# Optimization experiments

Hardware: AMD Instinct MI355X
Metric: run time of the kernel (lower is better)

Reference implementation:

```python
import math
import jax, jax.numpy as jnp
import numpy as np

B, T, C, H = 4, 1024, 1024, 16


def setup_inputs() -> dict:
    key = jax.random.key(0)
    k1, k2, k3 = jax.random.split(key, 3)
    scale = 0.02
    return {
        "x": jax.random.normal(k1, (B, T, C), dtype=jnp.float32),
        "w_attn": jax.random.normal(k2, (C, 3 * C), dtype=jnp.float32) * scale,
        "b_attn": jnp.zeros((3 * C,), dtype=jnp.float32),
        "w_proj": jax.random.normal(k3, (C, C), dtype=jnp.float32) * scale,
        "b_proj": jnp.zeros((C,), dtype=jnp.float32),
    }


def reference(x, w_attn, b_attn, w_proj, b_proj):
    b, t, c = x.shape
    h = H
    d = c // h
    qkv = x @ w_attn + b_attn                      # [b, t, 3c]
    q, k, v = jnp.split(qkv, 3, axis=-1)
    # [b, h, t, d]
    q = q.reshape(b, t, h, d).transpose(0, 2, 1, 3)
    k = k.reshape(b, t, h, d).transpose(0, 2, 1, 3)
    v = v.reshape(b, t, h, d).transpose(0, 2, 1, 3)
    att = jnp.einsum("bhqd,bhkd->bhqk", q, k) * (1.0 / math.sqrt(d))
    causal = jnp.tril(jnp.ones((t, t), dtype=bool))
    att = jnp.where(causal[None, None], att, -jnp.inf)
    att = jax.nn.softmax(att, axis=-1)
    # dropout is identity in eval mode
    y = jnp.einsum("bhqk,bhkd->bhqd", att, v)      # [b, h, t, d]
    y = y.transpose(0, 2, 1, 3).reshape(b, t, c)
    return y @ w_proj + b_proj
```

## Files before the change

### kernel.cpp

```cpp
#include <hip/hip_runtime.h>

typedef __bf16 bf16;
typedef float f32x4 __attribute__((ext_vector_type(4)));
typedef bf16 bf16x4 __attribute__((ext_vector_type(4)));
typedef bf16 bf16x8 __attribute__((ext_vector_type(8)));

#define MFMA16(a, b, c) __builtin_amdgcn_mfma_f32_16x16x32_bf16((a), (b), (c), 0, 0, 0)

__device__ __forceinline__ f32x4 zero4() {
    f32x4 z; z[0] = 0.f; z[1] = 0.f; z[2] = 0.f; z[3] = 0.f; return z;
}
__device__ __forceinline__ float max3f(float a, float b, float c) {
    return fmaxf(fmaxf(a, b), c);
}
__device__ __forceinline__ void gl_lds16(const bf16* g, bf16* l) {
    __builtin_amdgcn_global_load_lds(
        (const __attribute__((address_space(1))) void*)g,
        (__attribute__((address_space(3))) void*)l, 16, 0, 0);
}

__global__ __launch_bounds__(256)
void prep_k(const float* __restrict__ x, bf16* __restrict__ xb,
            const float* __restrict__ w_attn, bf16* __restrict__ wT,
            const float* __restrict__ w_proj, bf16* __restrict__ wpT)
{
    __shared__ bf16 Ls[64][72];
    const int blk = blockIdx.x;
    const int tid = threadIdx.x;

    if (blk < 2048) {
        const int i = (blk * 256 + tid) * 8;
        const float4 a = *(const float4*)(x + i);
        const float4 b = *(const float4*)(x + i + 4);
        bf16x8 o;
        o[0] = (bf16)a.x; o[1] = (bf16)a.y; o[2] = (bf16)a.z; o[3] = (bf16)a.w;
        o[4] = (bf16)b.x; o[5] = (bf16)b.y; o[6] = (bf16)b.z; o[7] = (bf16)b.w;
        *(bf16x8*)(xb + i) = o;
        return;
    }
    const float* src;
    bf16* dst;
    int K, N, bx, by;
    if (blk < 2816) {
        const int r = blk - 2048;
        src = w_attn; dst = wT; K = 1024; N = 3072;
        bx = r % 48; by = r / 48;
    } else {
        const int r = blk - 2816;
        src = w_proj; dst = wpT; K = 1024; N = 1024;
        bx = r & 15; by = r >> 4;
    }
    const int k0 = by << 6;
    const int n0 = bx << 6;
    #pragma unroll
    for (int it = 0; it < 4; ++it) {
        const int lin = (it << 10) + (tid << 2);
        const int r = lin >> 6, c = lin & 63;
        const float4 v = *(const float4*)(src + (size_t)(k0 + r) * N + n0 + c);
        bf16x4 o; o[0] = (bf16)v.x; o[1] = (bf16)v.y; o[2] = (bf16)v.z; o[3] = (bf16)v.w;
        *(bf16x4*)&Ls[r][c] = o;
    }
    __syncthreads();
    #pragma unroll
    for (int it = 0; it < 2; ++it) {
        const int lin = (it << 11) + (tid << 3);
        const int nn = lin >> 6, kk = lin & 63;
        bf16x8 o;
        #pragma unroll
        for (int j = 0; j < 8; ++j) o[j] = Ls[kk + j][nn];
        *(bf16x8*)(dst + (size_t)(n0 + nn) * K + k0 + kk) = o;
    }
}

template <int MODE>
__global__ __launch_bounds__(256)
void gemm_bt(const bf16* __restrict__ A, const bf16* __restrict__ Bt,
             const float* __restrict__ bias,
             bf16* __restrict__ qw, bf16* __restrict__ kw, bf16* __restrict__ vw,
             float* __restrict__ outf)
{
    constexpr int BK = 32;
    constexpr int BN = (MODE == 0) ? 128 : 64;
    constexpr int K  = 1024;
    constexpr int N  = (MODE == 0) ? 3072 : 1024;
    constexpr int MF = (MODE == 0) ? 4 : 2;
    constexpr int NF = 4;
    constexpr int AE = 128 * BK;
    constexpr int BE = BN * BK;
    constexpr int nk = K / BK;

    __shared__ __align__(16) bf16 smem[3 * (AE + BE)];
    bf16* const Asb = smem;
    bf16* const Bsb = smem + 3 * AE;

    const int tid  = threadIdx.x;
    const int lane = tid & 63;
    const int wid  = tid >> 6;
    const int l16  = lane & 15;
    const int g    = lane >> 4;
    const int wrb  = (MODE == 0) ? ((wid >> 1) << 6) : (wid << 5);
    const int wcb  = (MODE == 0) ? ((wid & 1) << 6) : 0;

    const int p   = blockIdx.x;
    const int xcd = p & 7;
    const int r   = p >> 3;
    int by, bx;
    if (MODE == 0) { by = ((xcd >> 1) << 3) + r / 12; bx = (xcd & 1) * 12 + r % 12; }
    else           { by = ((xcd >> 1) << 3) + (r >> 3); bx = ((xcd & 1) << 3) + (r & 7); }
    const int m0 = by << 7;
    const int n0 = bx * BN;

    const int srow = lane >> 2;
    const int schk = lane & 3;
    const int rA0 = (wid << 5) + srow;
    const int rA1 = rA0 + 16;
    const int rB0 = wid * (BN / 4) + srow;
    const int rB1 = rB0 + 16;
    const bf16* const pa0 = A  + (size_t)(m0 + rA0) * K + ((schk ^ ((rA0 >> 1) & 3)) << 3);
    const bf16* const pa1 = A  + (size_t)(m0 + rA1) * K + ((schk ^ ((rA1 >> 1) & 3)) << 3);
    const bf16* const pb0 = Bt + (size_t)(n0 + rB0) * K + ((schk ^ ((rB0 >> 1) & 3)) << 3);
    const bf16* const pb1 = Bt + (size_t)(n0 + rB1) * K + ((schk ^ ((rB1 >> 1) & 3)) << 3);
    const int dA0 = (wid << 5) * BK, dA1 = dA0 + 16 * BK;
    const int dB0 = (wid * (BN / 4)) * BK, dB1 = dB0 + 16 * BK;

    int offA[MF], offB[NF];
    #pragma unroll
    for (int mf = 0; mf < MF; ++mf) {
        const int rr = wrb + (mf << 4) + l16;
        offA[mf] = rr * BK + ((g ^ ((rr >> 1) & 3)) << 3);
    }
    #pragma unroll
    for (int nf = 0; nf < NF; ++nf) {
        const int rr = wcb + (nf << 4) + l16;
        offB[nf] = rr * BK + ((g ^ ((rr >> 1) & 3)) << 3);
    }

    f32x4 acc[MF][NF];
    #pragma unroll
    for (int i = 0; i < MF; ++i)
        #pragma unroll
        for (int j = 0; j < NF; ++j) acc[i][j] = zero4();

    auto issue = [&](int t, int s) {
        bf16* const ab = Asb + s * AE;
        bf16* const bb = Bsb + s * BE;
        gl_lds16(pa0 + t * BK, ab + dA0);
        gl_lds16(pa1 + t * BK, ab + dA1);
        gl_lds16(pb0 + t * BK, bb + dB0);
        if constexpr (MODE == 0) gl_lds16(pb1 + t * BK, bb + dB1);
    };

    issue(0, 0);
    issue(1, 1);

    #pragma unroll
    for (int kt = 0; kt < nk; ++kt) {
        if (kt == nk - 1) {
            asm volatile("s_waitcnt vmcnt(0)" ::: "memory");
        } else {
            if constexpr (MODE == 0) asm volatile("s_waitcnt vmcnt(4)" ::: "memory");
            else                     asm volatile("s_waitcnt vmcnt(3)" ::: "memory");
        }
        __builtin_amdgcn_s_barrier();
        if (kt + 2 < nk) issue(kt + 2, (kt + 2) % 3);
        const bf16* const ac = Asb + (kt % 3) * AE;
        const bf16* const bc = Bsb + (kt % 3) * BE;
        bf16x8 af[MF], bfr[NF];
        #pragma unroll
        for (int mf = 0; mf < MF; ++mf) af[mf] = *(const bf16x8*)&ac[offA[mf]];
        #pragma unroll
        for (int nf = 0; nf < NF; ++nf) bfr[nf] = *(const bf16x8*)&bc[offB[nf]];
        __builtin_amdgcn_s_setprio(1);
        #pragma unroll
        for (int mf = 0; mf < MF; ++mf)
            #pragma unroll
            for (int nf = 0; nf < NF; ++nf)
                acc[mf][nf] = MFMA16(af[mf], bfr[nf], acc[mf][nf]);
        __builtin_amdgcn_s_setprio(0);
    }
    __syncthreads();

    if (MODE == 0) {
        bf16* const Es = smem;
        const int bq  = m0 >> 10;
        const int tb  = m0 & 1023;
        const int hh0 = (n0 & 1023) >> 6;
        const bool isV = (n0 >= 2048);
        if (isV) {
            #pragma unroll
            for (int mf = 0; mf < MF; ++mf)
                #pragma unroll
                for (int nf = 0; nf < NF; ++nf) {
                    const int nn = wcb + (nf << 4) + l16;
                    const float bs = bias[n0 + nn];
                    bf16x4 pq;
                    #pragma unroll
                    for (int j = 0; j < 4; ++j) pq[j] = (bf16)(acc[mf][nf][j] + bs);
                    const int m = wrb + (mf << 4) + (g << 2);
                    const int pp = ((m >> 5) << 5) + (((m >> 2) & 3) << 3) + (((m >> 4) & 1) << 2);
                    *(bf16x4*)&Es[nn * 128 + pp] = pq;
                }
        } else {
            #pragma unroll
            for (int mf = 0; mf < MF; ++mf)
                #pragma unroll
                for (int nf = 0; nf < NF; ++nf) {
                    const int nn = wcb + (nf << 4) + l16;
                    const float bs = bias[n0 + nn];
                    #pragma unroll
                    for (int j = 0; j < 4; ++j) {
                        const int mm = wrb + (mf << 4) + (g << 2) + j;
                        Es[mm * 128 + nn] = (bf16)(acc[mf][nf][j] + bs);
                    }
                }
        }
        __syncthreads();
        #pragma unroll
        for (int it = 0; it < 8; ++it) {
            const int idx = (it << 8) + tid;
            const int row = idx >> 4, ch = idx & 15;
            const bf16x8 v = *(const bf16x8*)&Es[row * 128 + (ch << 3)];
            if (isV) {
                const int dd = row & 63, hh = hh0 + (row >> 6);
                *(bf16x8*)(vw + ((size_t)((bq << 4) + hh) << 16) + ((size_t)dd << 10)
                           + tb + (ch << 3)) = v;
            } else {
                const int t = tb + row;
                const int cc = ch << 3;
                const int hh = hh0 + (cc >> 6);
                bf16* const dst = (n0 < 1024) ? qw : kw;
                *(bf16x8*)(dst + ((size_t)((bq << 4) + hh) << 16) + ((size_t)t << 6)
                           + (cc & 63)) = v;
            }
        }
    } else {
        #pragma unroll
        for (int mf = 0; mf < MF; ++mf)
            #pragma unroll
            for (int nf = 0; nf < NF; ++nf) {
                const int ng = n0 + wcb + (nf << 4) + l16;
                const float bs = bias[ng];
                #pragma unroll
                for (int j = 0; j < 4; ++j) {
                    const int mg = m0 + wrb + (mf << 4) + (g << 2) + j;
                    outf[(size_t)mg * N + ng] = acc[mf][nf][j] + bs;
                }
            }
    }
}

__global__ __launch_bounds__(256)
void attn_k(const bf16* __restrict__ Qp, const bf16* __restrict__ Kp,
            const bf16* __restrict__ Vt, bf16* __restrict__ att)
{
    __shared__ __align__(16) bf16 Kls[3 * 64 * 64];
    __shared__ __align__(16) bf16 Vls[3 * 64 * 64];

    const int bh = blockIdx.x;
    const int bx = blockIdx.y;
    const int b  = bh >> 4, h = bh & 15;

    const int tid  = threadIdx.x;
    const int lane = tid & 63;
    const int wid  = tid >> 6;
    const int g    = lane >> 4;
    const int l16  = lane & 15;
    const int g8   = g << 3;

    const size_t hb = (size_t)bh << 16;
    const bf16* Qh = Qp + hb;
    const bf16* Kh = Kp + hb;
    const bf16* Vh = Vt + hb;

    const int srow = lane >> 3;
    const int sswz = ((lane & 7) ^ srow) << 3;
    const int kr0  = (wid << 4) + srow;
    const int kr1  = kr0 + 8;
    const int dst0 = (wid << 4) << 6;
    const int dst1 = ((wid << 4) + 8) << 6;

    int offKV[2][4];
    #pragma unroll
    for (int ks = 0; ks < 2; ++ks)
        #pragma unroll
        for (int cb = 0; cb < 4; ++cb) {
            const int r = (cb << 4) + l16;
            offKV[ks][cb] = (r << 6) + (((((ks << 2) + g)) ^ (r & 7)) << 3);
        }

    const float QSCALE = 0.125f * 1.44269504f;

    const int q1b = bx;
    const int q2b = 15 - bx;
    const int nkt = q2b;
    const int qloc = (wid << 4) + l16;

    const bf16* qp1 = Qh + ((size_t)((q1b << 6) + qloc) << 6) + g8;
    const bf16* qp2 = Qh + ((size_t)((q2b << 6) + qloc) << 6) + g8;
    bf16x8 q1f0 = *(const bf16x8*)qp1, q1f1 = *(const bf16x8*)(qp1 + 32);
    bf16x8 q2f0 = *(const bf16x8*)qp2, q2f1 = *(const bf16x8*)(qp2 + 32);
    #pragma unroll
    for (int e = 0; e < 8; ++e) {
        q1f0[e] = (bf16)(QSCALE * (float)q1f0[e]);
        q1f1[e] = (bf16)(QSCALE * (float)q1f1[e]);
        q2f0[e] = (bf16)(QSCALE * (float)q2f0[e]);
        q2f1[e] = (bf16)(QSCALE * (float)q2f1[e]);
    }

    f32x4 acc1[4], acc2[4];
    float m1 = -1e30f, l1 = 0.f, m2 = -1e30f, l2 = 0.f;
    #pragma unroll
    for (int i = 0; i < 4; ++i) { acc1[i] = zero4(); acc2[i] = zero4(); }

    auto stage = [&](int t, int s) {
        const int kv = t << 6;
        bf16* const Kn = Kls + s * 4096;
        bf16* const Vn = Vls + s * 4096;
        gl_lds16(Kh + ((size_t)(kv + kr0) << 6) + sswz, Kn + dst0);
        gl_lds16(Kh + ((size_t)(kv + kr1) << 6) + sswz, Kn + dst1);
        gl_lds16(Vh + ((size_t)kr0 << 10) + kv + sswz, Vn + dst0);
        gl_lds16(Vh + ((size_t)kr1 << 10) + kv + sswz, Vn + dst1);
    };

    stage(0, 0);
    stage(1, 1);

    for (int kt = 0; kt <= nkt; ++kt) {
        const int slot = kt % 3;
        if (kt + 2 <= nkt) {
            stage(kt + 2, (kt + 2) % 3);
            asm volatile("s_waitcnt vmcnt(8)" ::: "memory");
        } else if (kt + 1 <= nkt) {
            asm volatile("s_waitcnt vmcnt(4)" ::: "memory");
        } else {
            asm volatile("s_waitcnt vmcnt(0)" ::: "memory");
        }
        __builtin_amdgcn_s_barrier();
        const bf16* Kc = Kls + slot * 4096;
        const bf16* Vc = Vls + slot * 4096;

        bf16x8 kf[2][4], vf[2][4];
        #pragma unroll
        for (int ks = 0; ks < 2; ++ks)
            #pragma unroll
            for (int cb = 0; cb < 4; ++cb) {
                kf[ks][cb] = *(const bf16x8*)&Kc[offKV[ks][cb]];
                vf[ks][cb] = *(const bf16x8*)&Vc[offKV[ks][cb]];
            }

        {
            f32x4 sacc[4];
            #pragma unroll
            for (int cb = 0; cb < 4; ++cb) sacc[cb] = zero4();
            #pragma unroll
            for (int cb = 0; cb < 4; ++cb) sacc[cb] = MFMA16(kf[0][cb], q2f0, sacc[cb]);
            #pragma unroll
            for (int cb = 0; cb < 4; ++cb) sacc[cb] = MFMA16(kf[1][cb], q2f1, sacc[cb]);
            if (kt == q2b) {
                #pragma unroll
                for (int cb = 0; cb < 4; ++cb)
                    #pragma unroll
                    for (int j = 0; j < 4; ++j)
                        if (((cb << 4) + (g << 2) + j) > qloc) sacc[cb][j] = -1e30f;
            }
            const float t0 = max3f(sacc[0][0], sacc[0][1], sacc[0][2]);
            const float t1 = max3f(sacc[0][3], sacc[1][0], sacc[1][1]);
            const float t2 = max3f(sacc[1][2], sacc[1][3], sacc[2][0]);
            const float t3 = max3f(sacc[2][1], sacc[2][2], sacc[2][3]);
            const float t4 = max3f(sacc[3][0], sacc[3][1], sacc[3][2]);
            float pm = fmaxf(max3f(t0, t1, t2), max3f(t3, t4, sacc[3][3]));
            pm = fmaxf(pm, __shfl_xor(pm, 16));
            pm = fmaxf(pm, __shfl_xor(pm, 32));
            if (__any(pm > m2 + 8.f)) {
                const float mn = fmaxf(m2, pm);
                const float sc = __builtin_amdgcn_exp2f(m2 - mn);
                m2 = mn; l2 *= sc;
                #pragma unroll
                for (int db = 0; db < 4; ++db)
                    #pragma unroll
                    for (int j = 0; j < 4; ++j) acc2[db][j] *= sc;
            }
            float rsum = 0.f;
            #pragma unroll
            for (int cb = 0; cb < 4; ++cb)
                #pragma unroll
                for (int j = 0; j < 4; ++j) {
                    const float pv = __builtin_amdgcn_exp2f(sacc[cb][j] - m2);
                    sacc[cb][j] = pv;
                    rsum += pv;
                }
            rsum += __shfl_xor(rsum, 16);
            rsum += __shfl_xor(rsum, 32);
            l2 += rsum;
            bf16x8 pf0, pf1;
            #pragma unroll
            for (int i = 0; i < 8; ++i) {
                pf0[i] = (bf16)sacc[i >> 2][i & 3];
                pf1[i] = (bf16)sacc[2 + (i >> 2)][i & 3];
            }
            #pragma unroll
            for (int db = 0; db < 4; ++db) acc2[db] = MFMA16(vf[0][db], pf0, acc2[db]);
            #pragma unroll
            for (int db = 0; db < 4; ++db) acc2[db] = MFMA16(vf[1][db], pf1, acc2[db]);
        }

        if (kt <= q1b) {
            f32x4 sacc[4];
            #pragma unroll
            for (int cb = 0; cb < 4; ++cb) sacc[cb] = zero4();
            #pragma unroll
            for (int cb = 0; cb < 4; ++cb) sacc[cb] = MFMA16(kf[0][cb], q1f0, sacc[cb]);
            #pragma unroll
            for (int cb = 0; cb < 4; ++cb) sacc[cb] = MFMA16(kf[1][cb], q1f1, sacc[cb]);
            if (kt == q1b) {
                #pragma unroll
                for (int cb = 0; cb < 4; ++cb)
                    #pragma unroll
                    for (int j = 0; j < 4; ++j)
                        if (((cb << 4) + (g << 2) + j) > qloc) sacc[cb][j] = -1e30f;
            }
            const float t0 = max3f(sacc[0][0], sacc[0][1], sacc[0][2]);
            const float t1 = max3f(sacc[0][3], sacc[1][0], sacc[1][1]);
            const float t2 = max3f(sacc[1][2], sacc[1][3], sacc[2][0]);
            const float t3 = max3f(sacc[2][1], sacc[2][2], sacc[2][3]);
            const float t4 = max3f(sacc[3][0], sacc[3][1], sacc[3][2]);
            float pm = fmaxf(max3f(t0, t1, t2), max3f(t3, t4, sacc[3][3]));
            pm = fmaxf(pm, __shfl_xor(pm, 16));
            pm = fmaxf(pm, __shfl_xor(pm, 32));
            if (__any(pm > m1 + 8.f)) {
                const float mn = fmaxf(m1, pm);
                const float sc = __builtin_amdgcn_exp2f(m1 - mn);
                m1 = mn; l1 *= sc;
                #pragma unroll
                for (int db = 0; db < 4; ++db)
                    #pragma unroll
                    for (int j = 0; j < 4; ++j) acc1[db][j] *= sc;
            }
            float rsum = 0.f;
            #pragma unroll
            for (int cb = 0; cb < 4; ++cb)
                #pragma unroll
                for (int j = 0; j < 4; ++j) {
                    const float pv = __builtin_amdgcn_exp2f(sacc[cb][j] - m1);
                    sacc[cb][j] = pv;
                    rsum += pv;
                }
            rsum += __shfl_xor(rsum, 16);
            rsum += __shfl_xor(rsum, 32);
            l1 += rsum;
            bf16x8 pf0, pf1;
            #pragma unroll
            for (int i = 0; i < 8; ++i) {
                pf0[i] = (bf16)sacc[i >> 2][i & 3];
                pf1[i] = (bf16)sacc[2 + (i >> 2)][i & 3];
            }
            #pragma unroll
            for (int db = 0; db < 4; ++db) acc1[db] = MFMA16(vf[0][db], pf0, acc1[db]);
            #pragma unroll
            for (int db = 0; db < 4; ++db) acc1[db] = MFMA16(vf[1][db], pf1, acc1[db]);
        }
        asm volatile("" ::: "memory");
        __builtin_amdgcn_s_barrier();
        asm volatile("" ::: "memory");
    }

    {
        const float inv = 1.f / l2;
        const int t = (q2b << 6) + qloc;
        #pragma unroll
        for (int db = 0; db < 4; ++db) {
            bf16x4 o;
            #pragma unroll
            for (int j = 0; j < 4; ++j) o[j] = (bf16)(acc2[db][j] * inv);
            *(bf16x4*)(att + (((size_t)b << 10) + t) * 1024 + (h << 6) + (db << 4) + (g << 2)) = o;
        }
    }
    {
        const float inv = 1.f / l1;
        const int t = (q1b << 6) + qloc;
        #pragma unroll
        for (int db = 0; db < 4; ++db) {
            bf16x4 o;
            #pragma unroll
            for (int j = 0; j < 4; ++j) o[j] = (bf16)(acc1[db][j] * inv);
            *(bf16x4*)(att + (((size_t)b << 10) + t) * 1024 + (h << 6) + (db << 4) + (g << 2)) = o;
        }
    }
}

extern "C" void kernel_launch(void* const* d_in, const int* in_sizes, int n_in,
                              void* d_out, int out_size, void* d_ws, size_t ws_size,
                              hipStream_t stream)
{
    const float* x      = (const float*)d_in[0];
    const float* w_attn = (const float*)d_in[1];
    const float* b_attn = (const float*)d_in[2];
    const float* w_proj = (const float*)d_in[3];
    const float* b_proj = (const float*)d_in[4];
    float* out = (float*)d_out;

    bf16* xb  = (bf16*)d_ws;
    bf16* wT  = xb  + (size_t)4096 * 1024;
    bf16* wpT = wT  + (size_t)3072 * 1024;
    bf16* qw  = wpT + (size_t)1024 * 1024;
    bf16* kw  = qw  + (size_t)64 * 1024 * 64;
    bf16* vw  = kw  + (size_t)64 * 1024 * 64;
    bf16* aw  = vw  + (size_t)64 * 1024 * 64;

    prep_k<<<3072, 256, 0, stream>>>(x, xb, w_attn, wT, w_proj, wpT);

    gemm_bt<0><<<768, 256, 0, stream>>>(xb, wT, b_attn, qw, kw, vw, nullptr);
    attn_k<<<dim3(64, 8), 256, 0, stream>>>(qw, kw, vw, aw);
    gemm_bt<1><<<512, 256, 0, stream>>>(aw, wpT, b_proj, nullptr, nullptr, nullptr, out);
}
```

Measured before the change: 84.76 us.

## Split paired causal query blocks into one block per CTA with XCD-aware mapping

The attention kernel previously had each CTA handle a pair of query blocks (bx and 15-bx) that shared the K/V tiles loaded into LDS. It now launches 1024 CTAs, each owning a single 64-row query block. The CTA index is remapped so that each XCD gets whole heads and the longest query blocks are scheduled first. The K/V ring shrinks from three LDS stages to double buffering, which cuts LDS per CTA and should allow more CTAs per CU. The cost is that every K/V tile is loaded twice as often, with less reuse per load, and there is more per-CTA setup overhead.

```diff
diff --git a/kernel.cpp b/kernel.cpp
--- a/kernel.cpp
+++ b/kernel.cpp
@@ -253,12 +253,18 @@
 void attn_k(const bf16* __restrict__ Qp, const bf16* __restrict__ Kp,
             const bf16* __restrict__ Vt, bf16* __restrict__ att)
 {
-    __shared__ __align__(16) bf16 Kls[3 * 64 * 64];
-    __shared__ __align__(16) bf16 Vls[3 * 64 * 64];
-
-    const int bh = blockIdx.x;
-    const int bx = blockIdx.y;
-    const int b  = bh >> 4, h = bh & 15;
+    __shared__ __align__(16) bf16 Kl0[4096], Kl1[4096];
+    __shared__ __align__(16) bf16 Vl0[4096], Vl1[4096];
+
+    const int p   = blockIdx.x;
+    const int xcd = p & 7;
+    const int i   = p >> 3;
+    const int bh  = (xcd << 3) + (i & 7);
+    const int iq  = i >> 3;
+    const int a   = iq >> 2, qs = iq & 3;
+    const int qb  = (a == 0) ? (15 - qs) : (a == 1) ? (8 + qs)
+                  : (a == 2) ? (7 - qs) : qs;
+    const int b   = bh >> 4, h = bh & 15;
 
     const int tid  = threadIdx.x;
     const int lane = tid & 63;
@@ -289,55 +295,43 @@
         }
 
     const float QSCALE = 0.125f * 1.44269504f;
-
-    const int q1b = bx;
-    const int q2b = 15 - bx;
-    const int nkt = q2b;
     const int qloc = (wid << 4) + l16;
-
-    const bf16* qp1 = Qh + ((size_t)((q1b << 6) + qloc) << 6) + g8;
-    const bf16* qp2 = Qh + ((size_t)((q2b << 6) + qloc) << 6) + g8;
-    bf16x8 q1f0 = *(const bf16x8*)qp1, q1f1 = *(const bf16x8*)(qp1 + 32);
-    bf16x8 q2f0 = *(const bf16x8*)qp2, q2f1 = *(const bf16x8*)(qp2 + 32);
+    const int q0 = qb << 6;
+
+    const bf16* qp = Qh + ((size_t)(q0 + qloc) << 6) + g8;
+    bf16x8 qf0 = *(const bf16x8*)qp, qf1 = *(const bf16x8*)(qp + 32);
     #pragma unroll
     for (int e = 0; e < 8; ++e) {
-        q1f0[e] = (bf16)(QSCALE * (float)q1f0[e]);
-        q1f1[e] = (bf16)(QSCALE * (float)q1f1[e]);
-        q2f0[e] = (bf16)(QSCALE * (float)q2f0[e]);
-        q2f1[e] = (bf16)(QSCALE * (float)q2f1[e]);
-    }
-
-    f32x4 acc1[4], acc2[4];
-    float m1 = -1e30f, l1 = 0.f, m2 = -1e30f, l2 = 0.f;
-    #pragma unroll
-    for (int i = 0; i < 4; ++i) { acc1[i] = zero4(); acc2[i] = zero4(); }
-
-    auto stage = [&](int t, int s) {
+        qf0[e] = (bf16)(QSCALE * (float)qf0[e]);
+        qf1[e] = (bf16)(QSCALE * (float)qf1[e]);
+    }
+
+    f32x4 acc_o[4];
+    float m_r = -1e30f, l_r = 0.f;
+    #pragma unroll
+    for (int i2 = 0; i2 < 4; ++i2) acc_o[i2] = zero4();
+
+    auto stage = [&](int t, bf16* Kn, bf16* Vn) {
         const int kv = t << 6;
-        bf16* const Kn = Kls + s * 4096;
-        bf16* const Vn = Vls + s * 4096;
         gl_lds16(Kh + ((size_t)(kv + kr0) << 6) + sswz, Kn + dst0);
         gl_lds16(Kh + ((size_t)(kv + kr1) << 6) + sswz, Kn + dst1);
         gl_lds16(Vh + ((size_t)kr0 << 10) + kv + sswz, Vn + dst0);
         gl_lds16(Vh + ((size_t)kr1 << 10) + kv + sswz, Vn + dst1);
     };
 
-    stage(0, 0);
-    stage(1, 1);
-
-    for (int kt = 0; kt <= nkt; ++kt) {
-        const int slot = kt % 3;
-        if (kt + 2 <= nkt) {
-            stage(kt + 2, (kt + 2) % 3);
-            asm volatile("s_waitcnt vmcnt(8)" ::: "memory");
-        } else if (kt + 1 <= nkt) {
+    stage(0, Kl0, Vl0);
+
+    for (int kt = 0; kt <= qb; ++kt) {
+        const bool odd = kt & 1;
+        if (kt < qb) {
+            stage(kt + 1, odd ? Kl0 : Kl1, odd ? Vl0 : Vl1);
             asm volatile("s_waitcnt vmcnt(4)" ::: "memory");
         } else {
             asm volatile("s_waitcnt vmcnt(0)" ::: "memory");
         }
         __builtin_amdgcn_s_barrier();
-        const bf16* Kc = Kls + slot * 4096;
-        const bf16* Vc = Vls + slot * 4096;
+        const bf16* Kc = odd ? Kl1 : Kl0;
+        const bf16* Vc = odd ? Vl1 : Vl0;
 
         bf16x8 kf[2][4], vf[2][4];
         #pragma unroll
@@ -348,143 +342,73 @@
                 vf[ks][cb] = *(const bf16x8*)&Vc[offKV[ks][cb]];
             }
 
-        {
-            f32x4 sacc[4];
-            #pragma unroll
-            for (int cb = 0; cb < 4; ++cb) sacc[cb] = zero4();
-            #pragma unroll
-            for (int cb = 0; cb < 4; ++cb) sacc[cb] = MFMA16(kf[0][cb], q2f0, sacc[cb]);
-            #pragma unroll
-            for (int cb = 0; cb < 4; ++cb) sacc[cb] = MFMA16(kf[1][cb], q2f1, sacc[cb]);
-            if (kt == q2b) {
-                #pragma unroll
-                for (int cb = 0; cb < 4; ++cb)
-                    #pragma unroll
-                    for (int j = 0; j < 4; ++j)
-                        if (((cb << 4) + (g << 2) + j) > qloc) sacc[cb][j] = -1e30f;
-            }
-            const float t0 = max3f(sacc[0][0], sacc[0][1], sacc[0][2]);
-            const float t1 = max3f(sacc[0][3], sacc[1][0], sacc[1][1]);
-            const float t2 = max3f(sacc[1][2], sacc[1][3], sacc[2][0]);
-            const float t3 = max3f(sacc[2][1], sacc[2][2], sacc[2][3]);
-            const float t4 = max3f(sacc[3][0], sacc[3][1], sacc[3][2]);
-            float pm = fmaxf(max3f(t0, t1, t2), max3f(t3, t4, sacc[3][3]));
-            pm = fmaxf(pm, __shfl_xor(pm, 16));
-            pm = fmaxf(pm, __shfl_xor(pm, 32));
-            if (__any(pm > m2 + 8.f)) {
-                const float mn = fmaxf(m2, pm);
-                const float sc = __builtin_amdgcn_exp2f(m2 - mn);
-                m2 = mn; l2 *= sc;
-                #pragma unroll
-                for (int db = 0; db < 4; ++db)
-                    #pragma unroll
-                    for (int j = 0; j < 4; ++j) acc2[db][j] *= sc;
-            }
-            float rsum = 0.f;
+        f32x4 sacc[4];
+        #pragma unroll
+        for (int cb = 0; cb < 4; ++cb) sacc[cb] = zero4();
+        #pragma unroll
+        for (int cb = 0; cb < 4; ++cb) sacc[cb] = MFMA16(kf[0][cb], qf0, sacc[cb]);
+        #pragma unroll
+        for (int cb = 0; cb < 4; ++cb) sacc[cb] = MFMA16(kf[1][cb], qf1, sacc[cb]);
+        if (kt == qb) {
             #pragma unroll
             for (int cb = 0; cb < 4; ++cb)
                 #pragma unroll
-                for (int j = 0; j < 4; ++j) {
-                    const float pv = __builtin_amdgcn_exp2f(sacc[cb][j] - m2);
-                    sacc[cb][j] = pv;
-                    rsum += pv;
-                }
-            rsum += __shfl_xor(rsum, 16);
-            rsum += __shfl_xor(rsum, 32);
-            l2 += rsum;
-            bf16x8 pf0, pf1;
-            #pragma unroll
-            for (int i = 0; i < 8; ++i) {
-                pf0[i] = (bf16)sacc[i >> 2][i & 3];
-                pf1[i] = (bf16)sacc[2 + (i >> 2)][i & 3];
+                for (int j = 0; j < 4; ++j)
+                    if (((cb << 4) + (g << 2) + j) > qloc) sacc[cb][j] = -1e30f;
+        }
+        const float t0 = max3f(sacc[0][0], sacc[0][1], sacc[0][2]);
+        const float t1 = max3f(sacc[0][3], sacc[1][0], sacc[1][1]);
+        const float t2 = max3f(sacc[1][2], sacc[1][3], sacc[2][0]);
+        const float t3 = max3f(sacc[2][1], sacc[2][2], sacc[2][3]);
+        const float t4 = max3f(sacc[3][0], sacc[3][1], sacc[3][2]);
+        float pm = fmaxf(max3f(t0, t1, t2), max3f(t3, t4, sacc[3][3]));
+        pm = fmaxf(pm, __shfl_xor(pm, 16));
+        pm = fmaxf(pm, __shfl_xor(pm, 32));
+        if (__any(pm > m_r + 8.f)) {
+            const float mn = fmaxf(m_r, pm);
+            const float sc = __builtin_amdgcn_exp2f(m_r - mn);
+            m_r = mn; l_r *= sc;
+            #pragma unroll
+            for (int db = 0; db < 4; ++db)
+                #pragma unroll
+                for (int j = 0; j < 4; ++j) acc_o[db][j] *= sc;
+        }
+        float rsum = 0.f;
+        #pragma unroll
+        for (int cb = 0; cb < 4; ++cb)
+            #pragma unroll
+            for (int j = 0; j < 4; ++j) {
+                const float pv = __builtin_amdgcn_exp2f(sacc[cb][j] - m_r);
+                sacc[cb][j] = pv;
+                rsum += pv;
             }
-            #pragma unroll
-            for (int db = 0; db < 4; ++db) acc2[db] = MFMA16(vf[0][db], pf0, acc2[db]);
-            #pragma unroll
-            for (int db = 0; db < 4; ++db) acc2[db] = MFMA16(vf[1][db], pf1, acc2[db]);
-        }
-
-        if (kt <= q1b) {
-            f32x4 sacc[4];
-            #pragma unroll
-            for (int cb = 0; cb < 4; ++cb) sacc[cb] = zero4();
-            #pragma unroll
-            for (int cb = 0; cb < 4; ++cb) sacc[cb] = MFMA16(kf[0][cb], q1f0, sacc[cb]);
-            #pragma unroll
-            for (int cb = 0; cb < 4; ++cb) sacc[cb] = MFMA16(kf[1][cb], q1f1, sacc[cb]);
-            if (kt == q1b) {
-                #pragma unroll
-                for (int cb = 0; cb < 4; ++cb)
-                    #pragma unroll
-                    for (int j = 0; j < 4; ++j)
-                        if (((cb << 4) + (g << 2) + j) > qloc) sacc[cb][j] = -1e30f;
-            }
-            const float t0 = max3f(sacc[0][0], sacc[0][1], sacc[0][2]);
-            const float t1 = max3f(sacc[0][3], sacc[1][0], sacc[1][1]);
-            const float t2 = max3f(sacc[1][2], sacc[1][3], sacc[2][0]);
-            const float t3 = max3f(sacc[2][1], sacc[2][2], sacc[2][3]);
-            const float t4 = max3f(sacc[3][0], sacc[3][1], sacc[3][2]);
-            float pm = fmaxf(max3f(t0, t1, t2), max3f(t3, t4, sacc[3][3]));
-            pm = fmaxf(pm, __shfl_xor(pm, 16));
-            pm = fmaxf(pm, __shfl_xor(pm, 32));
-            if (__any(pm > m1 + 8.f)) {
-                const float mn = fmaxf(m1, pm);
-                const float sc = __builtin_amdgcn_exp2f(m1 - mn);
-                m1 = mn; l1 *= sc;
-                #pragma unroll
-                for (int db = 0; db < 4; ++db)
-                    #pragma unroll
-                    for (int j = 0; j < 4; ++j) acc1[db][j] *= sc;
-            }
-            float rsum = 0.f;
-            #pragma unroll
-            for (int cb = 0; cb < 4; ++cb)
-                #pragma unroll
-                for (int j = 0; j < 4; ++j) {
-                    const float pv = __builtin_amdgcn_exp2f(sacc[cb][j] - m1);
-                    sacc[cb][j] = pv;
-                    rsum += pv;
-                }
-            rsum += __shfl_xor(rsum, 16);
-            rsum += __shfl_xor(rsum, 32);
-            l1 += rsum;
-            bf16x8 pf0, pf1;
-            #pragma unroll
-            for (int i = 0; i < 8; ++i) {
-                pf0[i] = (bf16)sacc[i >> 2][i & 3];
-                pf1[i] = (bf16)sacc[2 + (i >> 2)][i & 3];
-            }
-            #pragma unroll
-            for (int db = 0; db < 4; ++db) acc1[db] = MFMA16(vf[0][db], pf0, acc1[db]);
-            #pragma unroll
-            for (int db = 0; db < 4; ++db) acc1[db] = MFMA16(vf[1][db], pf1, acc1[db]);
-        }
+        rsum += __shfl_xor(rsum, 16);
+        rsum += __shfl_xor(rsum, 32);
+        l_r += rsum;
+        bf16x8 pf0, pf1;
+        #pragma unroll
+        for (int e = 0; e < 8; ++e) {
+            pf0[e] = (bf16)sacc[e >> 2][e & 3];
+            pf1[e] = (bf16)sacc[2 + (e >> 2)][e & 3];
+        }
+        #pragma unroll
+        for (int db = 0; db < 4; ++db) acc_o[db] = MFMA16(vf[0][db], pf0, acc_o[db]);
+        #pragma unroll
+        for (int db = 0; db < 4; ++db) acc_o[db] = MFMA16(vf[1][db], pf1, acc_o[db]);
+
         asm volatile("" ::: "memory");
         __builtin_amdgcn_s_barrier();
         asm volatile("" ::: "memory");
     }
 
-    {
-        const float inv = 1.f / l2;
-        const int t = (q2b << 6) + qloc;
-        #pragma unroll
-        for (int db = 0; db < 4; ++db) {
-            bf16x4 o;
-            #pragma unroll
-            for (int j = 0; j < 4; ++j) o[j] = (bf16)(acc2[db][j] * inv);
-            *(bf16x4*)(att + (((size_t)b << 10) + t) * 1024 + (h << 6) + (db << 4) + (g << 2)) = o;
-        }
-    }
-    {
-        const float inv = 1.f / l1;
-        const int t = (q1b << 6) + qloc;
-        #pragma unroll
-        for (int db = 0; db < 4; ++db) {
-            bf16x4 o;
-            #pragma unroll
-            for (int j = 0; j < 4; ++j) o[j] = (bf16)(acc1[db][j] * inv);
-            *(bf16x4*)(att + (((size_t)b << 10) + t) * 1024 + (h << 6) + (db << 4) + (g << 2)) = o;
-        }
+    const float inv = 1.f / l_r;
+    const int t = q0 + qloc;
+    #pragma unroll
+    for (int db = 0; db < 4; ++db) {
+        bf16x4 o;
+        #pragma unroll
+        for (int j = 0; j < 4; ++j) o[j] = (bf16)(acc_o[db][j] * inv);
+        *(bf16x4*)(att + (((size_t)b << 10) + t) * 1024 + (h << 6) + (db << 4) + (g << 2)) = o;
     }
 }
 
@@ -510,6 +434,6 @@
     prep_k<<<3072, 256, 0, stream>>>(x, xb, w_attn, wT, w_proj, wpT);
 
     gemm_bt<0><<<768, 256, 0, stream>>>(xb, wT, b_attn, qw, kw, vw, nullptr);
-    attn_k<<<dim3(64, 8), 256, 0, stream>>>(qw, kw, vw, aw);
+    attn_k<<<1024, 256, 0, stream>>>(qw, kw, vw, aw);
     gemm_bt<1><<<512, 256, 0, stream>>>(aw, wpT, b_proj, nullptr, nullptr, nullptr, out);
 }
```

Measured after the change: 81.96 us (median of 2 runs). -3.3%, faster.
